# Kernel tuning notes

Measured on AMD Instinct MI355X. Metric: run time of the kernel, lower is better.

## Reference

```python
import jax, jax.numpy as jnp
import numpy as np

N_NODES = 50000
N_EDGES = 800000
N_GRAPHS = 64
F0 = 64          # num_features
HID = 512        # hidden_size
N_OUT = 1


def setup_inputs() -> dict:
    key = jax.random.key(0)
    ks = jax.random.split(key, 16)

    def p(k, shape, scale):
        return jax.random.normal(k, shape, jnp.float32) * scale

    inp = {}
    inp["feature"] = jax.random.normal(ks[0], (N_NODES, F0), jnp.float32)
    inp["edge_index"] = jax.random.randint(ks[1], (2, N_EDGES), 0, N_NODES)
    inp["protein_batch"] = jnp.sort(jax.random.randint(ks[2], (N_NODES,), 0, N_GRAPHS))

    dims = [(F0, F0), (F0, 2 * F0), (2 * F0, 4 * F0)]
    for i, (din, dout) in enumerate(dims):
        s = 1.0 / np.sqrt(din)
        inp[f"W{i+1}"] = p(ks[3 + 3 * i], (din, dout), s)      # GATConv lin weight
        inp[f"att{i+1}"] = p(ks[4 + 3 * i], (2, dout), 0.1)    # [att_src; att_dst]
        inp[f"b{i+1}"] = jnp.zeros((dout,), jnp.float32)       # GATConv bias
    inp["fc1_w"] = p(ks[12], (4 * F0, HID), 1.0 / np.sqrt(4 * F0))
    inp["fc1_b"] = jnp.zeros((HID,), jnp.float32)
    inp["fc2_w"] = p(ks[13], (HID, N_OUT), 1.0 / np.sqrt(HID))
    inp["fc2_b"] = jnp.zeros((N_OUT,), jnp.float32)
    return inp


def _gat_conv(x, src, dst, W, att, b):
    """PyG GATConv, heads=1, concat=True, negative_slope=0.2 (self-loops already in src/dst)."""
    h = x @ W                                             # [N, Dout]
    # per-edge attention logit: a_src . h_j + a_dst . h_i
    alpha = jax.nn.leaky_relu(h @ att[0], 0.2 * 0 + 0.0)  # placeholder, replaced below
    logit = jax.nn.leaky_relu((h @ att[0])[src] + (h @ att[1])[dst], negative_slope=0.2)  # [E]
    # segment softmax over edges grouped by destination node
    m = jax.ops.segment_max(logit, dst, num_segments=N_NODES)      # [N]
    e = jnp.exp(logit - m[dst])                                    # [E]
    s = jax.ops.segment_sum(e, dst, num_segments=N_NODES)          # [N]
    coef = e / s[dst]                                              # [E]
    out = jax.ops.segment_sum(coef[:, None] * h[src], dst, num_segments=N_NODES)  # [N, Dout]
    return out + b


def reference(feature, edge_index, protein_batch,
              W1, att1, b1, W2, att2, b2, W3, att3, b3,
              fc1_w, fc1_b, fc2_w, fc2_b):
    loop = jnp.arange(N_NODES)
    src = jnp.concatenate([edge_index[0], loop])   # add_self_loops=True
    dst = jnp.concatenate([edge_index[1], loop])

    x = jax.nn.relu(_gat_conv(feature, src, dst, W1, att1, b1))
    x = jax.nn.relu(_gat_conv(x, src, dst, W2, att2, b2))
    x = jax.nn.relu(_gat_conv(x, src, dst, W3, att3, b3))

    # global mean pool per graph
    sums = jax.ops.segment_sum(x, protein_batch, num_segments=N_GRAPHS)          # [G, 4F]
    cnts = jax.ops.segment_sum(jnp.ones((N_NODES,), x.dtype), protein_batch,
                               num_segments=N_GRAPHS)                            # [G]
    gc = sums / jnp.maximum(cnts, 1.0)[:, None]

    gc = jax.nn.relu(gc @ fc1_w + fc1_b)   # dropout is identity at inference
    return gc @ fc2_w + fc2_b
```

## Files before the change

kernel.cpp:

```cpp
#include <hip/hip_runtime.h>
#include <hip/hip_bf16.h>

#define N_NODES 50000
#define N_EDGES 800000
#define E_TOT   850000
#define N_GRAPHS 64
#define HID 512

typedef unsigned short u16;
typedef __attribute__((ext_vector_type(8))) short short8;
typedef __attribute__((ext_vector_type(4))) float floatx4;
typedef union { uint4 u; short8 s; } frag_u;

__device__ inline unsigned f2b(float x) {
    unsigned u = __float_as_uint(x);
    return (u + 0x7fffu + ((u >> 16) & 1u)) >> 16;
}
__device__ inline float b2f_lo(unsigned u) { return __uint_as_float(u << 16); }
__device__ inline float b2f_hi(unsigned u) { return __uint_as_float(u & 0xffff0000u); }

__global__ __launch_bounds__(256) void count_kernel(const int* __restrict__ dst_e,
                                                    int* __restrict__ cnt,
                                                    int* __restrict__ order) {
    int e = blockIdx.x * 256 + threadIdx.x;
    if (e >= E_TOT) return;
    int d = (e < N_EDGES) ? dst_e[e] : (e - N_EDGES);
    order[e] = atomicAdd(&cnt[d], 1);
}

__global__ __launch_bounds__(256) void scan_local(const int* __restrict__ cnt,
                                                  int* __restrict__ out,
                                                  int* __restrict__ blocksum, int n) {
    __shared__ int buf[256];
    int tid = threadIdx.x;
    int i = blockIdx.x * 256 + tid;
    int v = (i < n) ? cnt[i] : 0;
    buf[tid] = v;
    __syncthreads();
    for (int off = 1; off < 256; off <<= 1) {
        int t = (tid >= off) ? buf[tid - off] : 0;
        __syncthreads();
        buf[tid] += t;
        __syncthreads();
    }
    if (i < n) out[i] = buf[tid] - v;
    if (tid == 255) blocksum[blockIdx.x] = buf[255];
}

__global__ __launch_bounds__(256) void scan_block(const int* __restrict__ blocksum,
                                                  int* __restrict__ blockoff, int nb,
                                                  int* __restrict__ total_ptr) {
    __shared__ int buf[256];
    int tid = threadIdx.x;
    int v = (tid < nb) ? blocksum[tid] : 0;
    buf[tid] = v;
    __syncthreads();
    for (int off = 1; off < 256; off <<= 1) {
        int t = (tid >= off) ? buf[tid - off] : 0;
        __syncthreads();
        buf[tid] += t;
        __syncthreads();
    }
    blockoff[tid] = buf[tid] - v;
    if (tid == 255) *total_ptr = buf[255];
}

__global__ __launch_bounds__(256) void scan_add(int* __restrict__ row_ptr,
                                                const int* __restrict__ blockoff, int n) {
    int i = blockIdx.x * 256 + threadIdx.x;
    if (i < n) row_ptr[i] += blockoff[blockIdx.x];
}

__global__ __launch_bounds__(256) void fill_kernel(const int* __restrict__ edge_index,
                                                   const int* __restrict__ row_ptr,
                                                   const int* __restrict__ order,
                                                   int* __restrict__ col_idx) {
    int e = blockIdx.x * 256 + threadIdx.x;
    if (e >= E_TOT) return;
    int s, d;
    if (e < N_EDGES) { s = edge_index[e]; d = edge_index[N_EDGES + e]; }
    else             { s = e - N_EDGES;   d = s; }
    col_idx[row_ptr[d] + order[e]] = s;
}

struct PrepDesc {
    const float* W[3];
    const float* att[3];
    float* wsd[3];
    u16* Wt[3];
};

__global__ __launch_bounds__(256) void prep_kernel(PrepDesc d) {
    const int DIN[3]  = {64, 64, 128};
    const int DOUT[3] = {64, 128, 256};
    int b = blockIdx.x;
    if (b < 128) {
        int wg = (b * 256 + (int)threadIdx.x) >> 6;
        int lane = threadIdx.x & 63;
        int l = (wg < 128) ? 0 : (wg < 256) ? 1 : 2;
        int base = (l == 0) ? 0 : (l == 1) ? 128 : 256;
        int k = wg - base;
        int Din = DIN[l], Dout = DOUT[l];
        int half = (k >= Din) ? 1 : 0;
        int row = half ? (k - Din) : k;
        float s = 0.f;
        for (int j = lane; j < Dout; j += 64)
            s += d.W[l][(size_t)row * Dout + j] * d.att[l][half * Dout + j];
#pragma unroll
        for (int off = 32; off > 0; off >>= 1) s += __shfl_xor(s, off);
        if (lane == 0) d.wsd[l][k] = s;
    } else {
        int t = (b - 128) * 256 + (int)threadIdx.x;
        int l; int off;
        if (t < 4096)       { l = 0; off = t; }
        else if (t < 12288) { l = 1; off = t - 4096; }
        else if (t < 45056) { l = 2; off = t - 12288; }
        else return;
        int Din = DIN[l], Dout = DOUT[l];
        int row = off / Dout, j = off & (Dout - 1);
        d.Wt[l][(size_t)j * Din + row] = (u16)f2b(d.W[l][off]);
    }
}

__global__ __launch_bounds__(256) void cvt_lsld_kernel(const float* __restrict__ feature,
                                                       const float* __restrict__ wsd,
                                                       u16* __restrict__ Fb,
                                                       float* __restrict__ lsld) {
    int wid = (blockIdx.x * 256 + threadIdx.x) >> 6;
    int lane = threadIdx.x & 63;
    if (wid >= N_NODES) return;
    float h = feature[(size_t)wid * 64 + lane];
    float a0 = h * wsd[lane];
    float a1 = h * wsd[64 + lane];
#pragma unroll
    for (int off = 32; off > 0; off >>= 1) {
        a0 += __shfl_xor(a0, off);
        a1 += __shfl_xor(a1, off);
    }
    if (lane == 0) { lsld[wid] = a0; lsld[N_NODES + wid] = a1; }
    Fb[(size_t)wid * 64 + lane] = (u16)f2b(h);
}

template <int NN, int KK>
__global__ __launch_bounds__(256) void sgemm_mfma_kernel(const u16* __restrict__ A,
                                                         const u16* __restrict__ Bt,
                                                         u16* __restrict__ C,
                                                         const float* __restrict__ bias,
                                                         const float* __restrict__ wsd_next,
                                                         float* __restrict__ lsld_next,
                                                         int M) {
    constexpr int NT = 4;
    constexpr int KSTEPS = KK / 32;
    constexpr int CS = 72;
    __shared__ u16 cst[4][32 * CS];
    const int lane = threadIdx.x & 63;
    const int w = threadIdx.x >> 6;
    const int c = lane & 15;
    const int q = lane >> 4;
    const int bn = blockIdx.y * 64;
    const int r0 = blockIdx.x * 128 + w * 32;
    int ar0 = r0 + c;      if (ar0 > M - 1) ar0 = M - 1;
    int ar1 = r0 + 16 + c; if (ar1 > M - 1) ar1 = M - 1;
    const u16* __restrict__ Ap0 = A + (size_t)ar0 * KK + q * 8;
    const u16* __restrict__ Ap1 = A + (size_t)ar1 * KK + q * 8;
    floatx4 acc[2][NT];
#pragma unroll
    for (int i = 0; i < 2; ++i)
#pragma unroll
        for (int b = 0; b < NT; ++b) acc[i][b] = (floatx4){0.f, 0.f, 0.f, 0.f};
#pragma unroll
    for (int ks = 0; ks < KSTEPS; ++ks) {
        const int k0 = ks * 32;
        frag_u a0, a1, bf[NT];
        a0.u = *(const uint4*)(Ap0 + k0);
        a1.u = *(const uint4*)(Ap1 + k0);
#pragma unroll
        for (int b = 0; b < NT; ++b)
            bf[b].u = *(const uint4*)(Bt + (size_t)(bn + b * 16 + c) * KK + q * 8 + k0);
#pragma unroll
        for (int b = 0; b < NT; ++b) {
            acc[0][b] = __builtin_amdgcn_mfma_f32_16x16x32_bf16(a0.s, bf[b].s, acc[0][b], 0, 0, 0);
            acc[1][b] = __builtin_amdgcn_mfma_f32_16x16x32_bf16(a1.s, bf[b].s, acc[1][b], 0, 0, 0);
        }
    }
    const bool has_next = (wsd_next != nullptr);
    u16* __restrict__ cb = cst[w];
    float ps[2][4] = {}, pd[2][4] = {};
#pragma unroll
    for (int b = 0; b < NT; ++b) {
        const int col = bn + b * 16 + c;
        const float bsv = bias[col];
        const float wsv = has_next ? wsd_next[col] : 0.f;
        const float wdv = has_next ? wsd_next[NN + col] : 0.f;
#pragma unroll
        for (int i = 0; i < 2; ++i) {
#pragma unroll
            for (int g = 0; g < 4; ++g) {
                float v = fmaxf(acc[i][b][g] + bsv, 0.f);
                cb[(i * 16 + q * 4 + g) * CS + b * 16 + c] = (u16)f2b(v);
                ps[i][g] += v * wsv;
                pd[i][g] += v * wdv;
            }
        }
    }
    if (has_next) {
#pragma unroll
        for (int i = 0; i < 2; ++i)
#pragma unroll
            for (int g = 0; g < 4; ++g) {
#pragma unroll
                for (int mm = 1; mm < 16; mm <<= 1) {
                    ps[i][g] += __shfl_xor(ps[i][g], mm);
                    pd[i][g] += __shfl_xor(pd[i][g], mm);
                }
            }
        if (c == 0) {
#pragma unroll
            for (int i = 0; i < 2; ++i)
#pragma unroll
                for (int g = 0; g < 4; ++g) {
                    int r = r0 + i * 16 + q * 4 + g;
                    if (r < M) {
                        atomicAdd(&lsld_next[r], ps[i][g]);
                        atomicAdd(&lsld_next[M + r], pd[i][g]);
                    }
                }
        }
    }
#pragma unroll
    for (int p = 0; p < 4; ++p) {
        int lr = p * 8 + (lane >> 3);
        int r = r0 + lr;
        if (r < M) {
            uint4 val = *(const uint4*)&cb[lr * CS + (lane & 7) * 8];
            *(uint4*)(C + (size_t)r * NN + bn + (lane & 7) * 8) = val;
        }
    }
}

template <int D>
__global__ __launch_bounds__(256) void gather_fused_kernel(const u16* __restrict__ X,
                                                           const float* __restrict__ lsld,
                                                           const int* __restrict__ row_ptr,
                                                           const int* __restrict__ col_idx,
                                                           u16* __restrict__ out) {
    constexpr int L = D / 8;
    constexpr int P = 64 / L;
    __shared__ float2 ec_all[4][64];
    int wid = (blockIdx.x * 256 + threadIdx.x) >> 6;
    int lane = threadIdx.x & 63;
    if (wid >= N_NODES) return;
    float2* __restrict__ ec = ec_all[threadIdx.x >> 6];
    const int start = row_ptr[wid];
    const int end = row_ptr[wid + 1];
    const int deg = end - start;
    const float ldi = lsld[N_NODES + wid];
    const float* __restrict__ ls = lsld;
    const int eslot = lane / L;
    const int fidx = lane % L;
    float a[8] = {0.f, 0.f, 0.f, 0.f, 0.f, 0.f, 0.f, 0.f};

    auto fma8 = [&](float cc, uint4 v) {
        a[0] += cc * b2f_lo(v.x); a[1] += cc * b2f_hi(v.x);
        a[2] += cc * b2f_lo(v.y); a[3] += cc * b2f_hi(v.y);
        a[4] += cc * b2f_lo(v.z); a[5] += cc * b2f_hi(v.z);
        a[6] += cc * b2f_lo(v.w); a[7] += cc * b2f_hi(v.w);
    };

    if (deg <= 64) {
        int srcl = 0;
        float l = -3.0e38f;
        if (lane < deg) {
            srcl = col_idx[start + lane];
            float t = ls[srcl] + ldi;
            l = (t > 0.f) ? t : 0.2f * t;
        }
        float m = l;
#pragma unroll
        for (int off = 32; off > 0; off >>= 1) m = fmaxf(m, __shfl_xor(m, off));
        float e = (lane < deg) ? __expf(l - m) : 0.f;
        float s = e;
#pragma unroll
        for (int off = 32; off > 0; off >>= 1) s += __shfl_xor(s, off);
        ec[lane] = make_float2(e / s, __int_as_float(srcl));

        const int nsteps = (deg + P - 1) / P;
        for (int g0 = 0; g0 < nsteps; g0 += 4) {
            float2 p[4]; uint4 v[4];
#pragma unroll
            for (int j = 0; j < 4; ++j) {
                int idx = (g0 + j) * P + eslot;
                bool valid = idx < deg;
                p[j] = ec[valid ? idx : 0];
                if (!valid) p[j].x = 0.f;
            }
#pragma unroll
            for (int j = 0; j < 4; ++j)
                v[j] = *(const uint4*)(X + (size_t)__float_as_int(p[j].y) * D + fidx * 8);
#pragma unroll
            for (int j = 0; j < 4; ++j) fma8(p[j].x, v[j]);
        }
    } else {
        float m = -3.0e38f;
        for (int e = start + lane; e < end; e += 64) {
            float t = ls[col_idx[e]] + ldi;
            t = (t > 0.f) ? t : 0.2f * t;
            m = fmaxf(m, t);
        }
#pragma unroll
        for (int off = 32; off > 0; off >>= 1) m = fmaxf(m, __shfl_xor(m, off));
        float ssum = 0.f;
        for (int e = start + lane; e < end; e += 64) {
            float t = ls[col_idx[e]] + ldi;
            t = (t > 0.f) ? t : 0.2f * t;
            ssum += __expf(t - m);
        }
#pragma unroll
        for (int off = 32; off > 0; off >>= 1) ssum += __shfl_xor(ssum, off);
        const float inv = 1.0f / ssum;
        for (int e0 = start; e0 < end; e0 += P) {
            int e = e0 + eslot;
            if (e < end) {
                int src = col_idx[e];
                float t = ls[src] + ldi;
                t = (t > 0.f) ? t : 0.2f * t;
                float cc = __expf(t - m) * inv;
                uint4 v = *(const uint4*)(X + (size_t)src * D + fidx * 8);
                fma8(cc, v);
            }
        }
    }
#pragma unroll
    for (int mm = L; mm < 64; mm <<= 1) {
#pragma unroll
        for (int i = 0; i < 8; ++i) a[i] += __shfl_xor(a[i], mm);
    }
    if (lane < L) {
        uint4 o;
        o.x = f2b(a[0]) | (f2b(a[1]) << 16);
        o.y = f2b(a[2]) | (f2b(a[3]) << 16);
        o.z = f2b(a[4]) | (f2b(a[5]) << 16);
        o.w = f2b(a[6]) | (f2b(a[7]) << 16);
        *(uint4*)(out + (size_t)wid * D + lane * 8) = o;
    }
}

__device__ inline int lower_bound_dev(const int* __restrict__ a, int n, int v) {
    int lo = 0, hi = n;
    while (lo < hi) { int mid = (lo + hi) >> 1; if (a[mid] < v) lo = mid + 1; else hi = mid; }
    return lo;
}

#define POOL_SPLITS 32
__global__ __launch_bounds__(256) void pool_kernel(const u16* __restrict__ x3,
                                                   const int* __restrict__ batch,
                                                   float* __restrict__ gsum,
                                                   int* __restrict__ gcnt) {
    int g = blockIdx.x;
    int split = blockIdx.y;
    int tid = threadIdx.x;
    int start = lower_bound_dev(batch, N_NODES, g);
    int end = lower_bound_dev(batch, N_NODES, g + 1);
    int nodes = end - start;
    int n0 = start + (int)((long long)nodes * split / POOL_SPLITS);
    int n1 = start + (int)((long long)nodes * (split + 1) / POOL_SPLITS);
    float acc = 0.f;
    for (int n = n0; n < n1; ++n) acc += b2f_lo((unsigned)x3[(size_t)n * 256 + tid]);
    atomicAdd(&gsum[g * 256 + tid], acc);
    if (split == 0 && tid == 0) gcnt[g] = nodes;
}

__global__ __launch_bounds__(256) void fc_kernel(const float* __restrict__ gsum,
                                                 const int* __restrict__ gcnt,
                                                 const float* __restrict__ w1,
                                                 const float* __restrict__ b1,
                                                 const float* __restrict__ w2,
                                                 const float* __restrict__ b2,
                                                 float* __restrict__ out) {
    __shared__ float gc[256];
    __shared__ float h1s[HID];
    __shared__ float red[256];
    int g = blockIdx.x;
    int tid = threadIdx.x;
    float denom = fmaxf((float)gcnt[g], 1.0f);
    gc[tid] = gsum[g * 256 + tid] / denom;
    __syncthreads();
#pragma unroll
    for (int jj = 0; jj < 2; ++jj) {
        int j = tid + jj * 256;
        float sum = b1[j];
        for (int k = 0; k < 256; ++k) sum += gc[k] * w1[k * HID + j];
        h1s[j] = (sum > 0.f) ? sum : 0.f;
    }
    __syncthreads();
    float acc = h1s[tid] * w2[tid] + h1s[tid + 256] * w2[tid + 256];
    red[tid] = acc;
    __syncthreads();
    for (int off = 128; off > 0; off >>= 1) {
        if (tid < off) red[tid] += red[tid + off];
        __syncthreads();
    }
    if (tid == 0) out[g] = red[0] + b2[0];
}

extern "C" void kernel_launch(void* const* d_in, const int* in_sizes, int n_in,
                              void* d_out, int out_size, void* d_ws, size_t ws_size,
                              hipStream_t stream) {
    const float* feature  = (const float*)d_in[0];
    const int*   edge_idx = (const int*)d_in[1];
    const int*   batch    = (const int*)d_in[2];
    const float* W1    = (const float*)d_in[3];
    const float* att1  = (const float*)d_in[4];
    const float* b1    = (const float*)d_in[5];
    const float* W2    = (const float*)d_in[6];
    const float* att2  = (const float*)d_in[7];
    const float* b2    = (const float*)d_in[8];
    const float* W3    = (const float*)d_in[9];
    const float* att3  = (const float*)d_in[10];
    const float* b3    = (const float*)d_in[11];
    const float* fc1_w = (const float*)d_in[12];
    const float* fc1_b = (const float*)d_in[13];
    const float* fc2_w = (const float*)d_in[14];
    const float* fc2_b = (const float*)d_in[15];
    float* out = (float*)d_out;

    char* w = (char*)d_ws;
    auto alloc = [&](size_t bytes) {
        char* p = w;
        w += (bytes + 255) & ~(size_t)255;
        return p;
    };
    u16* Fb    = (u16*)alloc((size_t)N_NODES * 64 * 2);
    u16* X1b   = (u16*)alloc((size_t)N_NODES * 64 * 2);
    u16* X2b   = (u16*)alloc((size_t)N_NODES * 128 * 2);
    u16* X3b   = (u16*)alloc((size_t)N_NODES * 256 * 2);
    u16* AGGb  = (u16*)alloc((size_t)N_NODES * 128 * 2);
    float* lsld1 = (float*)alloc((size_t)N_NODES * 2 * 4);
    char* zbase = w;
    int* cnt      = (int*)alloc((size_t)N_NODES * 4);
    float* gsum   = (float*)alloc(64 * 256 * 4);
    float* lsld23 = (float*)alloc((size_t)N_NODES * 4 * 4);
    size_t zbytes = (size_t)(w - zbase);
    float* lsld2 = lsld23;
    float* lsld3 = lsld23 + (size_t)N_NODES * 2;
    float* wsd1  = (float*)alloc(2 * 64 * 4);
    float* wsd2  = (float*)alloc(2 * 64 * 4);
    float* wsd3  = (float*)alloc(2 * 128 * 4);
    u16* Wt1   = (u16*)alloc(64 * 64 * 2);
    u16* Wt2   = (u16*)alloc(128 * 64 * 2);
    u16* Wt3   = (u16*)alloc(256 * 128 * 2);
    int* row_ptr  = (int*)alloc((size_t)(N_NODES + 1) * 4);
    int* col_idx  = (int*)alloc((size_t)E_TOT * 4);
    int* order    = (int*)alloc((size_t)E_TOT * 4);
    int* blocksum = (int*)alloc(256 * 4);
    int* blockoff = (int*)alloc(256 * 4);
    int* gcnt     = (int*)alloc(64 * 4);

    hipMemsetAsync(zbase, 0, zbytes, stream);

    const int EB = (E_TOT + 255) / 256;
    const int NB = (N_NODES + 255) / 256;
    const int WB = (N_NODES * 64 + 255) / 256;
    const int GB = (N_NODES + 127) / 128;

    PrepDesc pd;
    pd.W[0] = W1; pd.W[1] = W2; pd.W[2] = W3;
    pd.att[0] = att1; pd.att[1] = att2; pd.att[2] = att3;
    pd.wsd[0] = wsd1; pd.wsd[1] = wsd2; pd.wsd[2] = wsd3;
    pd.Wt[0] = Wt1; pd.Wt[1] = Wt2; pd.Wt[2] = Wt3;
    prep_kernel<<<304, 256, 0, stream>>>(pd);

    count_kernel<<<EB, 256, 0, stream>>>(edge_idx + N_EDGES, cnt, order);
    scan_local<<<NB, 256, 0, stream>>>(cnt, row_ptr, blocksum, N_NODES);
    scan_block<<<1, 256, 0, stream>>>(blocksum, blockoff, NB, row_ptr + N_NODES);
    scan_add<<<NB, 256, 0, stream>>>(row_ptr, blockoff, N_NODES);
    fill_kernel<<<EB, 256, 0, stream>>>(edge_idx, row_ptr, order, col_idx);

    cvt_lsld_kernel<<<WB, 256, 0, stream>>>(feature, wsd1, Fb, lsld1);
    gather_fused_kernel<64><<<WB, 256, 0, stream>>>(Fb, lsld1, row_ptr, col_idx, AGGb);
    sgemm_mfma_kernel<64, 64><<<dim3(GB, 1), 256, 0, stream>>>(AGGb, Wt1, X1b, b1, wsd2, lsld2, N_NODES);

    gather_fused_kernel<64><<<WB, 256, 0, stream>>>(X1b, lsld2, row_ptr, col_idx, AGGb);
    sgemm_mfma_kernel<128, 64><<<dim3(GB, 2), 256, 0, stream>>>(AGGb, Wt2, X2b, b2, wsd3, lsld3, N_NODES);

    gather_fused_kernel<128><<<WB, 256, 0, stream>>>(X2b, lsld3, row_ptr, col_idx, AGGb);
    sgemm_mfma_kernel<256, 128><<<dim3(GB, 4), 256, 0, stream>>>(AGGb, Wt3, X3b, b3, nullptr, nullptr, N_NODES);

    pool_kernel<<<dim3(N_GRAPHS, POOL_SPLITS), 256, 0, stream>>>(X3b, batch, gsum, gcnt);
    fc_kernel<<<N_GRAPHS, 256, 0, stream>>>(gsum, gcnt, fc1_w, fc1_b, fc2_w, fc2_b, out);
}
```

Measured before the change: 318.3 us.

## Fuse global mean pooling into final GEMM epilogue and drop pool kernel

The last GAT layer's GEMM epilogue now applies bias and ReLU and accumulates per-graph column sums directly into gsum with atomics, instead of writing the N×256 bf16 activation and rereading it in a separate pool kernel. Warps whose 32 rows all belong to one graph reduce across lanes first, and mixed warps flush per-graph partial sums. Node counts per graph are now computed in fc_kernel by binary search. This removes a large write and read plus one launch, but adds many atomics and skips bf16 rounding of X3, which changes numerics slightly.

```diff
diff --git a/kernel.cpp b/kernel.cpp
--- a/kernel.cpp
+++ b/kernel.cpp
@@ -148,6 +148,8 @@
                                                          const float* __restrict__ bias,
                                                          const float* __restrict__ wsd_next,
                                                          float* __restrict__ lsld_next,
+                                                         const int* __restrict__ batch,
+                                                         float* __restrict__ gsum_pool,
                                                          int M) {
     constexpr int NT = 4;
     constexpr int KSTEPS = KK / 32;
@@ -183,6 +185,60 @@
             acc[1][b] = __builtin_amdgcn_mfma_f32_16x16x32_bf16(a1.s, bf[b].s, acc[1][b], 0, 0, 0);
         }
     }
+
+    if (gsum_pool) {
+        float bsv[NT];
+#pragma unroll
+        for (int b = 0; b < NT; ++b) bsv[b] = bias[bn + b * 16 + c];
+        const bool full = (r0 + 31 < M);
+        const int rl = full ? (r0 + 31) : (M - 1);
+        if (full && batch[r0] == batch[rl]) {
+            const int gr = batch[r0];
+#pragma unroll
+            for (int b = 0; b < NT; ++b) {
+                float s = 0.f;
+#pragma unroll
+                for (int i = 0; i < 2; ++i)
+#pragma unroll
+                    for (int g = 0; g < 4; ++g) s += fmaxf(acc[i][b][g] + bsv[b], 0.f);
+                s += __shfl_xor(s, 16);
+                s += __shfl_xor(s, 32);
+                if (q == 0) atomicAdd(&gsum_pool[gr * 256 + bn + b * 16 + c], s);
+            }
+        } else {
+#pragma unroll
+            for (int i = 0; i < 2; ++i) {
+                int curg = -1;
+                float sb[NT] = {0.f, 0.f, 0.f, 0.f};
+#pragma unroll
+                for (int g = 0; g < 4; ++g) {
+                    int r = r0 + i * 16 + q * 4 + g;
+                    if (r < M) {
+                        int gr = batch[r];
+                        if (gr != curg) {
+                            if (curg >= 0) {
+#pragma unroll
+                                for (int b = 0; b < NT; ++b) {
+                                    atomicAdd(&gsum_pool[curg * 256 + bn + b * 16 + c], sb[b]);
+                                    sb[b] = 0.f;
+                                }
+                            }
+                            curg = gr;
+                        }
+#pragma unroll
+                        for (int b = 0; b < NT; ++b) sb[b] += fmaxf(acc[i][b][g] + bsv[b], 0.f);
+                    }
+                }
+                if (curg >= 0) {
+#pragma unroll
+                    for (int b = 0; b < NT; ++b)
+                        atomicAdd(&gsum_pool[curg * 256 + bn + b * 16 + c], sb[b]);
+                }
+            }
+        }
+        return;
+    }
+
     const bool has_next = (wsd_next != nullptr);
     u16* __restrict__ cb = cst[w];
     float ps[2][4] = {}, pd[2][4] = {};
@@ -351,27 +407,8 @@
     return lo;
 }
 
-#define POOL_SPLITS 32
-__global__ __launch_bounds__(256) void pool_kernel(const u16* __restrict__ x3,
-                                                   const int* __restrict__ batch,
-                                                   float* __restrict__ gsum,
-                                                   int* __restrict__ gcnt) {
-    int g = blockIdx.x;
-    int split = blockIdx.y;
-    int tid = threadIdx.x;
-    int start = lower_bound_dev(batch, N_NODES, g);
-    int end = lower_bound_dev(batch, N_NODES, g + 1);
-    int nodes = end - start;
-    int n0 = start + (int)((long long)nodes * split / POOL_SPLITS);
-    int n1 = start + (int)((long long)nodes * (split + 1) / POOL_SPLITS);
-    float acc = 0.f;
-    for (int n = n0; n < n1; ++n) acc += b2f_lo((unsigned)x3[(size_t)n * 256 + tid]);
-    atomicAdd(&gsum[g * 256 + tid], acc);
-    if (split == 0 && tid == 0) gcnt[g] = nodes;
-}
-
 __global__ __launch_bounds__(256) void fc_kernel(const float* __restrict__ gsum,
-                                                 const int* __restrict__ gcnt,
+                                                 const int* __restrict__ batch,
                                                  const float* __restrict__ w1,
                                                  const float* __restrict__ b1,
                                                  const float* __restrict__ w2,
@@ -380,9 +417,13 @@
     __shared__ float gc[256];
     __shared__ float h1s[HID];
     __shared__ float red[256];
+    __shared__ int s_cnt;
     int g = blockIdx.x;
     int tid = threadIdx.x;
-    float denom = fmaxf((float)gcnt[g], 1.0f);
+    if (tid == 0)
+        s_cnt = lower_bound_dev(batch, N_NODES, g + 1) - lower_bound_dev(batch, N_NODES, g);
+    __syncthreads();
+    float denom = fmaxf((float)s_cnt, 1.0f);
     gc[tid] = gsum[g * 256 + tid] / denom;
     __syncthreads();
 #pragma unroll
@@ -433,7 +474,6 @@
     u16* Fb    = (u16*)alloc((size_t)N_NODES * 64 * 2);
     u16* X1b   = (u16*)alloc((size_t)N_NODES * 64 * 2);
     u16* X2b   = (u16*)alloc((size_t)N_NODES * 128 * 2);
-    u16* X3b   = (u16*)alloc((size_t)N_NODES * 256 * 2);
     u16* AGGb  = (u16*)alloc((size_t)N_NODES * 128 * 2);
     float* lsld1 = (float*)alloc((size_t)N_NODES * 2 * 4);
     char* zbase = w;
@@ -454,7 +494,6 @@
     int* order    = (int*)alloc((size_t)E_TOT * 4);
     int* blocksum = (int*)alloc(256 * 4);
     int* blockoff = (int*)alloc(256 * 4);
-    int* gcnt     = (int*)alloc(64 * 4);
 
     hipMemsetAsync(zbase, 0, zbytes, stream);
 
@@ -478,14 +517,13 @@
 
     cvt_lsld_kernel<<<WB, 256, 0, stream>>>(feature, wsd1, Fb, lsld1);
     gather_fused_kernel<64><<<WB, 256, 0, stream>>>(Fb, lsld1, row_ptr, col_idx, AGGb);
-    sgemm_mfma_kernel<64, 64><<<dim3(GB, 1), 256, 0, stream>>>(AGGb, Wt1, X1b, b1, wsd2, lsld2, N_NODES);
+    sgemm_mfma_kernel<64, 64><<<dim3(GB, 1), 256, 0, stream>>>(AGGb, Wt1, X1b, b1, wsd2, lsld2, nullptr, nullptr, N_NODES);
 
     gather_fused_kernel<64><<<WB, 256, 0, stream>>>(X1b, lsld2, row_ptr, col_idx, AGGb);
-    sgemm_mfma_kernel<128, 64><<<dim3(GB, 2), 256, 0, stream>>>(AGGb, Wt2, X2b, b2, wsd3, lsld3, N_NODES);
+    sgemm_mfma_kernel<128, 64><<<dim3(GB, 2), 256, 0, stream>>>(AGGb, Wt2, X2b, b2, wsd3, lsld3, nullptr, nullptr, N_NODES);
 
     gather_fused_kernel<128><<<WB, 256, 0, stream>>>(X2b, lsld3, row_ptr, col_idx, AGGb);
-    sgemm_mfma_kernel<256, 128><<<dim3(GB, 4), 256, 0, stream>>>(AGGb, Wt3, X3b, b3, nullptr, nullptr, N_NODES);
-
-    pool_kernel<<<dim3(N_GRAPHS, POOL_SPLITS), 256, 0, stream>>>(X3b, batch, gsum, gcnt);
-    fc_kernel<<<N_GRAPHS, 256, 0, stream>>>(gsum, gcnt, fc1_w, fc1_b, fc2_w, fc2_b, out);
-}
+    sgemm_mfma_kernel<256, 128><<<dim3(GB, 4), 256, 0, stream>>>(AGGb, Wt3, nullptr, b3, nullptr, nullptr, batch, gsum, N_NODES);
+
+    fc_kernel<<<N_GRAPHS, 256, 0, stream>>>(gsum, batch, fc1_w, fc1_b, fc2_w, fc2_b, out);
+}
```

Result: faster. 304.4 us (-4.4%).
